# Kernel tuning notes

Measured on AMD Instinct MI355X. Metric: run time of the kernel, lower is better.

The kernel has to match this reference:

```python
import jax, jax.numpy as jnp
import numpy as np

N, M, B, C, L, H = 8192, 8192, 16, 512, 64, 8
HEAD_DIM = C // H
PER_BATCH_KEYS = M // B
MASK_VAL = -1000.0  # matches torch masked_fill_ value


def setup_inputs() -> dict:
    key0 = jax.random.key(0)
    ks = jax.random.split(key0, 8)
    query = jax.random.normal(ks[0], (N, C), jnp.float32)
    key = jax.random.normal(ks[1], (M, C), jnp.float32)
    value = jax.random.normal(ks[2], (M, C), jnp.float32)
    # xavier-ish init for projections
    in_proj_weight = jax.random.normal(ks[3], (3 * C, C), jnp.float32) * (1.0 / np.sqrt(C))
    in_proj_bias = jnp.zeros((3 * C,), jnp.float32)
    out_w = jax.random.normal(ks[4], (C, C), jnp.float32) * (1.0 / np.sqrt(C))
    out_b = jnp.zeros((C,), jnp.float32)
    index_pair = jax.random.randint(ks[5], (N, L), 0, PER_BATCH_KEYS).astype(jnp.int32)
    pad = jax.random.uniform(ks[6], (N, L)) < 0.05
    index_pair = jnp.where(pad, jnp.int32(-1), index_pair)
    query_batch_cnt = jnp.full((B,), N // B, jnp.int32)
    key_batch_cnt = jnp.full((B,), PER_BATCH_KEYS, jnp.int32)
    index_pair_batch = jnp.repeat(jnp.arange(B, dtype=jnp.int32), N // B)
    return {
        "query": query, "key": key, "value": value,
        "in_proj_weight": in_proj_weight, "in_proj_bias": in_proj_bias,
        "out_w": out_w, "out_b": out_b,
        "index_pair": index_pair, "query_batch_cnt": query_batch_cnt,
        "key_batch_cnt": key_batch_cnt, "index_pair_batch": index_pair_batch,
    }


def reference(query, key, value, in_proj_weight, in_proj_bias, out_w, out_b,
              index_pair, query_batch_cnt, key_batch_cnt, index_pair_batch):
    embed_dim = query.shape[-1]
    scaling = float(HEAD_DIM) ** -0.5
    # qkv projections (in_proj_weight is [3C, C], applied as F.linear => x @ W.T + b)
    q = (query @ in_proj_weight[:embed_dim].T + in_proj_bias[:embed_dim]) * scaling
    k = key @ in_proj_weight[embed_dim:2 * embed_dim].T + in_proj_bias[embed_dim:2 * embed_dim]
    v = value @ in_proj_weight[2 * embed_dim:].T + in_proj_bias[2 * embed_dim:]
    q = q.reshape(N, H, HEAD_DIM)
    k = k.reshape(M, H, HEAD_DIM)
    v = v.reshape(M, H, HEAD_DIM)
    # local -> global key indices: offset by start of each query's batch key block
    key_start = jnp.cumsum(key_batch_cnt) - key_batch_cnt          # (B,)
    offset = key_start[index_pair_batch]                            # (N,)
    valid = index_pair >= 0                                         # (N, L)
    gidx = jnp.where(valid, index_pair + offset[:, None], 0)        # (N, L), safe gather
    # gather-based scores: (N, L, H)
    scores = jnp.einsum("nhd,nlhd->nlh", q, k[gidx])
    scores = jnp.where(valid[..., None], scores, MASK_VAL)
    w = jax.nn.softmax(scores, axis=1)                              # softmax over neighbors L
    # weighted value sum; masked weights underflow to exactly 0 in fp32
    attn = jnp.einsum("nlh,nlhd->nhd", w, v[gidx]).reshape(N, embed_dim)
    attn = attn @ out_w.T + out_b
    return attn, w.sum(axis=-1) / H
```

## Files before the change

kernel.cpp:

```cpp
#include <hip/hip_runtime.h>
#include <hip/hip_bf16.h>
#include <math.h>

#define NQ 8192
#define MK 8192
#define CD 512
#define LN 64
#define HH 8
#define HD 64
#define BB 16

typedef short short8 __attribute__((ext_vector_type(8)));
typedef float floatx4 __attribute__((ext_vector_type(4)));

__device__ __forceinline__ unsigned short f2bf(float x) {
    unsigned int u = __builtin_bit_cast(unsigned int, x);
    return (unsigned short)((u + 0x7FFFu + ((u >> 16) & 1u)) >> 16);
}
__device__ __forceinline__ unsigned int pkbf(float lo, float hi) {
    float2 f; f.x = lo; f.y = hi;
    __hip_bfloat162 h2 = __float22bfloat162_rn(f);
    unsigned int u;
    __builtin_memcpy(&u, &h2, 4);
    return u;
}
__device__ __forceinline__ float bflo(unsigned int u) {
    return __builtin_bit_cast(float, u << 16);
}
__device__ __forceinline__ float bfhi(unsigned int u) {
    return __builtin_bit_cast(float, u & 0xffff0000u);
}

__device__ __forceinline__ void gl_lds16(const unsigned short* g, unsigned short* l) {
    __builtin_amdgcn_global_load_lds(
        (const __attribute__((address_space(1))) unsigned int*)g,
        (__attribute__((address_space(3))) unsigned int*)l, 16, 0, 0);
}

struct ConvSeg { const float* src; unsigned short* dst; int n4; };
struct ConvArgs { ConvSeg s[5]; };

__global__ __launch_bounds__(256) void convert_bf16(ConvArgs a) {
    const int seg = blockIdx.y;
    const int i = blockIdx.x * 256 + threadIdx.x;
    if (i >= a.s[seg].n4) return;
    const float4 v = ((const float4*)a.s[seg].src)[i];
    uint2 o; o.x = pkbf(v.x, v.y); o.y = pkbf(v.z, v.w);
    ((uint2*)a.s[seg].dst)[i] = o;
}

__device__ __forceinline__ void gemm_bf_body(const unsigned short* __restrict__ A,
                                             const unsigned short* __restrict__ W,
                                             const float* __restrict__ bias,
                                             float* __restrict__ outf,
                                             unsigned short* __restrict__ outb,
                                             float scale) {
    __shared__ unsigned short As[128 * 64];
    __shared__ unsigned short Bs[128 * 64];

    const int tid  = threadIdx.x;
    const int row0 = blockIdx.x * 128;
    const int col0 = blockIdx.y * 128;

    const int w    = tid >> 6;
    const int lane = tid & 63;
    const int wr   = w >> 1;
    const int wc   = w & 1;
    const int q    = lane >> 4;
    const int ml   = lane & 15;

    const int sr = lane >> 3;
    const int sg = (lane & 7) ^ sr;
    const unsigned short* Ap = A + (size_t)(row0 + w * 32 + sr) * CD + sg * 8;
    const unsigned short* Wp = W + (size_t)(col0 + w * 32 + sr) * CD + sg * 8;
    unsigned short* Asw = &As[(w * 32) * 64];
    unsigned short* Bsw = &Bs[(w * 32) * 64];

    floatx4 acc[4][4];
#pragma unroll
    for (int i = 0; i < 4; ++i)
#pragma unroll
        for (int j = 0; j < 4; ++j)
            acc[i][j] = (floatx4){0.f, 0.f, 0.f, 0.f};

    for (int k0 = 0; k0 < CD; k0 += 64) {
        __syncthreads();
#pragma unroll
        for (int i = 0; i < 4; ++i) {
            gl_lds16(Ap + (size_t)(i * 8) * CD + k0, Asw + i * 8 * 64);
            gl_lds16(Wp + (size_t)(i * 8) * CD + k0, Bsw + i * 8 * 64);
        }
        __syncthreads();

#pragma unroll
        for (int kw = 0; kw < 2; ++kw) {
            short8 af[4], bf[4];
            const int gp = ((kw * 4 + q) ^ (ml & 7)) * 8;
#pragma unroll
            for (int mi = 0; mi < 4; ++mi)
                af[mi] = *(const short8*)&As[(wr * 64 + mi * 16 + ml) * 64 + gp];
#pragma unroll
            for (int ni = 0; ni < 4; ++ni)
                bf[ni] = *(const short8*)&Bs[(wc * 64 + ni * 16 + ml) * 64 + gp];
#pragma unroll
            for (int mi = 0; mi < 4; ++mi)
#pragma unroll
                for (int ni = 0; ni < 4; ++ni)
                    acc[mi][ni] = __builtin_amdgcn_mfma_f32_16x16x32_bf16(
                        af[mi], bf[ni], acc[mi][ni], 0, 0, 0);
        }
    }

    float bv[4];
#pragma unroll
    for (int ni = 0; ni < 4; ++ni)
        bv[ni] = bias[col0 + wc * 64 + ni * 16 + ml];
#pragma unroll
    for (int mi = 0; mi < 4; ++mi) {
#pragma unroll
        for (int ni = 0; ni < 4; ++ni) {
            const int cg = col0 + wc * 64 + ni * 16 + ml;
#pragma unroll
            for (int r = 0; r < 4; ++r) {
                const int rg = row0 + wr * 64 + mi * 16 + q * 4 + r;
                const float val = acc[mi][ni][r] + bv[ni];
                if (outb) outb[(size_t)rg * CD + cg] = f2bf(val);
                else      outf[(size_t)rg * CD + cg] = val * scale;
            }
        }
    }
}

__global__ __launch_bounds__(256) void qkv_gemm(const unsigned short* __restrict__ A_bf,
                                                const unsigned short* __restrict__ w_bf,
                                                const float* __restrict__ bias,
                                                float* __restrict__ q_ws,
                                                unsigned short* __restrict__ k_bf,
                                                unsigned short* __restrict__ v_bf) {
    const int z = blockIdx.z;
    const unsigned short* A = A_bf + (size_t)z * NQ * CD;
    float* outf = (z == 0) ? q_ws : nullptr;
    unsigned short* outb = (z == 1) ? k_bf : ((z == 2) ? v_bf : nullptr);
    gemm_bf_body(A, w_bf + (size_t)z * CD * CD, bias + (size_t)z * CD,
                 outf, outb, 0.125f);
}

__global__ __launch_bounds__(256) void out_gemm(const unsigned short* __restrict__ A,
                                                const unsigned short* __restrict__ W,
                                                const float* __restrict__ bias,
                                                float* __restrict__ out) {
    gemm_bf_body(A, W, bias, out, nullptr, 1.0f);
}

__global__ __launch_bounds__(512) void attn_kernel(
    const float* __restrict__ q_ws,
    const unsigned short* __restrict__ k_bf,
    const unsigned short* __restrict__ v_bf,
    const int* __restrict__ index_pair,
    const int* __restrict__ key_batch_cnt,
    const int* __restrict__ index_pair_batch,
    unsigned short* __restrict__ attn_bf,
    float* __restrict__ out2) {
    const int j = blockIdx.x;
    const int n = (j & 7) * (NQ / 8) + (j >> 3);

    const int tid  = threadIdx.x;
    const int h    = tid >> 6;
    const int lane = tid & 63;
    const int r    = lane >> 3;
    const int dg   = lane & 7;

    __shared__ float qs[CD];
    __shared__ float wmat[HH][LN];
    __shared__ int   gs[LN];

    qs[tid] = q_ws[(size_t)n * CD + tid];

    if (tid < LN) {
        const int batch = index_pair_batch[n];
        int offset = 0;
        for (int b = 0; b < batch; ++b) offset += key_batch_cnt[b];
        const int gi = index_pair[n * LN + tid];
        gs[tid] = (gi >= 0) ? (gi + offset) : 0;
    }
    __syncthreads();

    float q8[8];
#pragma unroll
    for (int d = 0; d < 8; ++d) q8[d] = qs[h * HD + dg * 8 + d];

    unsigned int off[8];
#pragma unroll
    for (int it = 0; it < 8; ++it)
        off[it] = (unsigned int)gs[it * 8 + r] * (CD * 2) + h * (HD * 2) + dg * 16;

#pragma unroll
    for (int it = 0; it < 8; ++it) {
        const uint4 kv = *(const uint4*)((const char*)k_bf + off[it]);
        float acc;
        acc  = bflo(kv.x) * q8[0];
        acc  = fmaf(bfhi(kv.x), q8[1], acc);
        acc  = fmaf(bflo(kv.y), q8[2], acc);
        acc  = fmaf(bfhi(kv.y), q8[3], acc);
        acc  = fmaf(bflo(kv.z), q8[4], acc);
        acc  = fmaf(bfhi(kv.z), q8[5], acc);
        acc  = fmaf(bflo(kv.w), q8[6], acc);
        acc  = fmaf(bfhi(kv.w), q8[7], acc);
        acc += __shfl_xor(acc, 1, 64);
        acc += __shfl_xor(acc, 2, 64);
        acc += __shfl_xor(acc, 4, 64);
        if (dg == 0) wmat[h][it * 8 + r] = acc;
    }

    float score = wmat[h][lane];
    if (index_pair[n * LN + lane] < 0) score = -1000.0f;
    float mx = score;
#pragma unroll
    for (int o = 32; o > 0; o >>= 1) mx = fmaxf(mx, __shfl_xor(mx, o, 64));
    float e = __expf(score - mx);
    float s = e;
#pragma unroll
    for (int o = 32; o > 0; o >>= 1) s += __shfl_xor(s, o, 64);
    const float w = e / s;
    wmat[h][lane] = w;
    __syncthreads();

    float a8[8] = {0.f, 0.f, 0.f, 0.f, 0.f, 0.f, 0.f, 0.f};
#pragma unroll
    for (int it = 0; it < 8; ++it) {
        const float wl = __shfl(w, it * 8 + r, 64);
        const uint4 vv = *(const uint4*)((const char*)v_bf + off[it]);
        a8[0] = fmaf(wl, bflo(vv.x), a8[0]);
        a8[1] = fmaf(wl, bfhi(vv.x), a8[1]);
        a8[2] = fmaf(wl, bflo(vv.y), a8[2]);
        a8[3] = fmaf(wl, bfhi(vv.y), a8[3]);
        a8[4] = fmaf(wl, bflo(vv.z), a8[4]);
        a8[5] = fmaf(wl, bfhi(vv.z), a8[5]);
        a8[6] = fmaf(wl, bflo(vv.w), a8[6]);
        a8[7] = fmaf(wl, bfhi(vv.w), a8[7]);
    }
#pragma unroll
    for (int o = 8; o <= 32; o <<= 1)
#pragma unroll
        for (int d = 0; d < 8; ++d) a8[d] += __shfl_xor(a8[d], o, 64);
    attn_bf[(size_t)n * CD + h * HD + dg * 8 + r] = f2bf(a8[r]);

    if (tid < LN) {
        float s8 = 0.f;
#pragma unroll
        for (int hh = 0; hh < HH; ++hh) s8 += wmat[hh][tid];
        out2[(size_t)n * LN + tid] = s8 * (1.0f / HH);
    }
}

extern "C" void kernel_launch(void* const* d_in, const int* in_sizes, int n_in,
                              void* d_out, int out_size, void* d_ws, size_t ws_size,
                              hipStream_t stream) {
    const float* query   = (const float*)d_in[0];
    const float* key     = (const float*)d_in[1];
    const float* value   = (const float*)d_in[2];
    const float* ipw     = (const float*)d_in[3];
    const float* ipb     = (const float*)d_in[4];
    const float* out_w   = (const float*)d_in[5];
    const float* out_b   = (const float*)d_in[6];
    const int*   index_pair       = (const int*)d_in[7];
    const int*   key_batch_cnt    = (const int*)d_in[9];
    const int*   index_pair_batch = (const int*)d_in[10];

    float* out = (float*)d_out;
    float* ws  = (float*)d_ws;
    float*          q_ws  = ws;
    unsigned short* k_bf  = (unsigned short*)(ws + (size_t)NQ * CD);
    unsigned short* v_bf  = k_bf + (size_t)NQ * CD;
    unsigned short* A_bf  = v_bf + (size_t)NQ * CD;
    unsigned short* w_bf  = A_bf + (size_t)3 * NQ * CD;
    unsigned short* ow_bf = w_bf + (size_t)3 * CD * CD;
    unsigned short* attn_bf = A_bf;

    ConvArgs ca;
    ca.s[0] = {query, A_bf,                      NQ * CD / 4};
    ca.s[1] = {key,   A_bf + (size_t)NQ * CD,    NQ * CD / 4};
    ca.s[2] = {value, A_bf + (size_t)2 * NQ * CD, NQ * CD / 4};
    ca.s[3] = {ipw,   w_bf,                      3 * CD * CD / 4};
    ca.s[4] = {out_w, ow_bf,                     CD * CD / 4};
    dim3 g0(NQ * CD / 4 / 256, 5);
    convert_bf16<<<g0, 256, 0, stream>>>(ca);

    dim3 g1(NQ / 128, CD / 128, 3);
    qkv_gemm<<<g1, 256, 0, stream>>>(A_bf, w_bf, ipb, q_ws, k_bf, v_bf);

    attn_kernel<<<NQ, 512, 0, stream>>>(q_ws, k_bf, v_bf, index_pair,
                                        key_batch_cnt, index_pair_batch,
                                        attn_bf, out + (size_t)NQ * CD);

    dim3 g3(NQ / 128, CD / 128, 1);
    out_gemm<<<g3, 256, 0, stream>>>(attn_bf, ow_bf, out_b, out);
}
```

Before: 230.9 us.

## Compute gathered QK scores with MFMA and store Q in bf16

The Q projection now writes bf16 instead of fp32, with the scale applied before rounding. The attention kernel computes each head's 64 gathered-key scores with two 16x16x32 bf16 MFMAs per 16-key group, instead of scalar FMAs plus three cross-lane shuffles. The high-half bf16 unpack in the value loop now skips masking the low bits. The aim is to cut Q memory traffic and the ALU and shuffle work in the score phase. In exchange, Q is rounded to bf16, and the value unpack carries small extra mantissa noise.

```diff
diff --git a/kernel.cpp b/kernel.cpp
--- a/kernel.cpp
+++ b/kernel.cpp
@@ -27,8 +27,11 @@
 __device__ __forceinline__ float bflo(unsigned int u) {
     return __builtin_bit_cast(float, u << 16);
 }
-__device__ __forceinline__ float bfhi(unsigned int u) {
-    return __builtin_bit_cast(float, u & 0xffff0000u);
+__device__ __forceinline__ float bfhij(unsigned int u) {
+    return __builtin_bit_cast(float, u);
+}
+__device__ __forceinline__ short8 u4s8(uint4 u) {
+    short8 s; __builtin_memcpy(&s, &u, 16); return s;
 }
 
 __device__ __forceinline__ void gl_lds16(const unsigned short* g, unsigned short* l) {
@@ -123,9 +126,9 @@
 #pragma unroll
             for (int r = 0; r < 4; ++r) {
                 const int rg = row0 + wr * 64 + mi * 16 + q * 4 + r;
-                const float val = acc[mi][ni][r] + bv[ni];
+                const float val = (acc[mi][ni][r] + bv[ni]) * scale;
                 if (outb) outb[(size_t)rg * CD + cg] = f2bf(val);
-                else      outf[(size_t)rg * CD + cg] = val * scale;
+                else      outf[(size_t)rg * CD + cg] = val;
             }
         }
     }
@@ -134,15 +137,14 @@
 __global__ __launch_bounds__(256) void qkv_gemm(const unsigned short* __restrict__ A_bf,
                                                 const unsigned short* __restrict__ w_bf,
                                                 const float* __restrict__ bias,
-                                                float* __restrict__ q_ws,
+                                                unsigned short* __restrict__ q_bf,
                                                 unsigned short* __restrict__ k_bf,
                                                 unsigned short* __restrict__ v_bf) {
     const int z = blockIdx.z;
     const unsigned short* A = A_bf + (size_t)z * NQ * CD;
-    float* outf = (z == 0) ? q_ws : nullptr;
-    unsigned short* outb = (z == 1) ? k_bf : ((z == 2) ? v_bf : nullptr);
+    unsigned short* outb = (z == 0) ? q_bf : ((z == 1) ? k_bf : v_bf);
     gemm_bf_body(A, w_bf + (size_t)z * CD * CD, bias + (size_t)z * CD,
-                 outf, outb, 0.125f);
+                 nullptr, outb, (z == 0) ? 0.125f : 1.0f);
 }
 
 __global__ __launch_bounds__(256) void out_gemm(const unsigned short* __restrict__ A,
@@ -153,7 +155,7 @@
 }
 
 __global__ __launch_bounds__(512) void attn_kernel(
-    const float* __restrict__ q_ws,
+    const unsigned short* __restrict__ q_bf,
     const unsigned short* __restrict__ k_bf,
     const unsigned short* __restrict__ v_bf,
     const int* __restrict__ index_pair,
@@ -167,14 +169,11 @@
     const int tid  = threadIdx.x;
     const int h    = tid >> 6;
     const int lane = tid & 63;
-    const int r    = lane >> 3;
-    const int dg   = lane & 7;
-
-    __shared__ float qs[CD];
+    const int quad = lane >> 4;
+    const int ml   = lane & 15;
+
     __shared__ float wmat[HH][LN];
     __shared__ int   gs[LN];
-
-    qs[tid] = q_ws[(size_t)n * CD + tid];
 
     if (tid < LN) {
         const int batch = index_pair_batch[n];
@@ -185,31 +184,29 @@
     }
     __syncthreads();
 
-    float q8[8];
-#pragma unroll
-    for (int d = 0; d < 8; ++d) q8[d] = qs[h * HD + dg * 8 + d];
-
-    unsigned int off[8];
-#pragma unroll
-    for (int it = 0; it < 8; ++it)
-        off[it] = (unsigned int)gs[it * 8 + r] * (CD * 2) + h * (HD * 2) + dg * 16;
-
-#pragma unroll
-    for (int it = 0; it < 8; ++it) {
-        const uint4 kv = *(const uint4*)((const char*)k_bf + off[it]);
-        float acc;
-        acc  = bflo(kv.x) * q8[0];
-        acc  = fmaf(bfhi(kv.x), q8[1], acc);
-        acc  = fmaf(bflo(kv.y), q8[2], acc);
-        acc  = fmaf(bfhi(kv.y), q8[3], acc);
-        acc  = fmaf(bflo(kv.z), q8[4], acc);
-        acc  = fmaf(bfhi(kv.z), q8[5], acc);
-        acc  = fmaf(bflo(kv.w), q8[6], acc);
-        acc  = fmaf(bfhi(kv.w), q8[7], acc);
-        acc += __shfl_xor(acc, 1, 64);
-        acc += __shfl_xor(acc, 2, 64);
-        acc += __shfl_xor(acc, 4, 64);
-        if (dg == 0) wmat[h][it * 8 + r] = acc;
+    const char* qp = (const char*)q_bf + (size_t)n * (CD * 2) + h * (HD * 2) + quad * 16;
+    const short8 bq0 = u4s8(*(const uint4*)qp);
+    const short8 bq1 = u4s8(*(const uint4*)(qp + 64));
+
+    int gr[4];
+#pragma unroll
+    for (int g = 0; g < 4; ++g) gr[g] = gs[g * 16 + ml];
+    uint4 a0[4], a1[4];
+#pragma unroll
+    for (int g = 0; g < 4; ++g) {
+        const char* kp = (const char*)k_bf + (size_t)gr[g] * (CD * 2) + h * (HD * 2) + quad * 16;
+        a0[g] = *(const uint4*)kp;
+        a1[g] = *(const uint4*)(kp + 64);
+    }
+#pragma unroll
+    for (int g = 0; g < 4; ++g) {
+        floatx4 sa = (floatx4){0.f, 0.f, 0.f, 0.f};
+        sa = __builtin_amdgcn_mfma_f32_16x16x32_bf16(u4s8(a0[g]), bq0, sa, 0, 0, 0);
+        sa = __builtin_amdgcn_mfma_f32_16x16x32_bf16(u4s8(a1[g]), bq1, sa, 0, 0, 0);
+        if (ml == 0) {
+#pragma unroll
+            for (int r = 0; r < 4; ++r) wmat[h][g * 16 + quad * 4 + r] = sa[r];
+        }
     }
 
     float score = wmat[h][lane];
@@ -225,19 +222,26 @@
     wmat[h][lane] = w;
     __syncthreads();
 
+    const int r  = lane >> 3;
+    const int dg = lane & 7;
+    unsigned int off[8];
+#pragma unroll
+    for (int it = 0; it < 8; ++it)
+        off[it] = (unsigned int)gs[it * 8 + r] * (CD * 2) + h * (HD * 2) + dg * 16;
+
     float a8[8] = {0.f, 0.f, 0.f, 0.f, 0.f, 0.f, 0.f, 0.f};
 #pragma unroll
     for (int it = 0; it < 8; ++it) {
         const float wl = __shfl(w, it * 8 + r, 64);
         const uint4 vv = *(const uint4*)((const char*)v_bf + off[it]);
-        a8[0] = fmaf(wl, bflo(vv.x), a8[0]);
-        a8[1] = fmaf(wl, bfhi(vv.x), a8[1]);
-        a8[2] = fmaf(wl, bflo(vv.y), a8[2]);
-        a8[3] = fmaf(wl, bfhi(vv.y), a8[3]);
-        a8[4] = fmaf(wl, bflo(vv.z), a8[4]);
-        a8[5] = fmaf(wl, bfhi(vv.z), a8[5]);
-        a8[6] = fmaf(wl, bflo(vv.w), a8[6]);
-        a8[7] = fmaf(wl, bfhi(vv.w), a8[7]);
+        a8[0] = fmaf(wl, bflo(vv.x),  a8[0]);
+        a8[1] = fmaf(wl, bfhij(vv.x), a8[1]);
+        a8[2] = fmaf(wl, bflo(vv.y),  a8[2]);
+        a8[3] = fmaf(wl, bfhij(vv.y), a8[3]);
+        a8[4] = fmaf(wl, bflo(vv.z),  a8[4]);
+        a8[5] = fmaf(wl, bfhij(vv.z), a8[5]);
+        a8[6] = fmaf(wl, bflo(vv.w),  a8[6]);
+        a8[7] = fmaf(wl, bfhij(vv.w), a8[7]);
     }
 #pragma unroll
     for (int o = 8; o <= 32; o <<= 1)
@@ -268,9 +272,8 @@
     const int*   index_pair_batch = (const int*)d_in[10];
 
     float* out = (float*)d_out;
-    float* ws  = (float*)d_ws;
-    float*          q_ws  = ws;
-    unsigned short* k_bf  = (unsigned short*)(ws + (size_t)NQ * CD);
+    unsigned short* q_bf  = (unsigned short*)d_ws;
+    unsigned short* k_bf  = q_bf + (size_t)NQ * CD;
     unsigned short* v_bf  = k_bf + (size_t)NQ * CD;
     unsigned short* A_bf  = v_bf + (size_t)NQ * CD;
     unsigned short* w_bf  = A_bf + (size_t)3 * NQ * CD;
@@ -278,18 +281,18 @@
     unsigned short* attn_bf = A_bf;
 
     ConvArgs ca;
-    ca.s[0] = {query, A_bf,                      NQ * CD / 4};
-    ca.s[1] = {key,   A_bf + (size_t)NQ * CD,    NQ * CD / 4};
+    ca.s[0] = {query, A_bf,                       NQ * CD / 4};
+    ca.s[1] = {key,   A_bf + (size_t)NQ * CD,     NQ * CD / 4};
     ca.s[2] = {value, A_bf + (size_t)2 * NQ * CD, NQ * CD / 4};
-    ca.s[3] = {ipw,   w_bf,                      3 * CD * CD / 4};
-    ca.s[4] = {out_w, ow_bf,                     CD * CD / 4};
+    ca.s[3] = {ipw,   w_bf,                       3 * CD * CD / 4};
+    ca.s[4] = {out_w, ow_bf,                      CD * CD / 4};
     dim3 g0(NQ * CD / 4 / 256, 5);
     convert_bf16<<<g0, 256, 0, stream>>>(ca);
 
     dim3 g1(NQ / 128, CD / 128, 3);
-    qkv_gemm<<<g1, 256, 0, stream>>>(A_bf, w_bf, ipb, q_ws, k_bf, v_bf);
-
-    attn_kernel<<<NQ, 512, 0, stream>>>(q_ws, k_bf, v_bf, index_pair,
+    qkv_gemm<<<g1, 256, 0, stream>>>(A_bf, w_bf, ipb, q_bf, k_bf, v_bf);
+
+    attn_kernel<<<NQ, 512, 0, stream>>>(q_bf, k_bf, v_bf, index_pair,
                                         key_batch_cnt, index_pair_batch,
                                         attn_bf, out + (size_t)NQ * CD);
 
```

Result: no change. 233.2 us (+1.0%).
